# Kernel optimization log

Measured on AMD Instinct MI355X. Metric: run time of the kernel, lower is better.

Reference implementation:

```python
import jax, jax.numpy as jnp
import numpy as np

B, C, D, O = 64, 64, 512, 256
N_REG, G = 8, 8  # 8 regions of 8 channels


def setup_inputs() -> dict:
    key = jax.random.key(0)
    ks = jax.random.split(key, 9)
    std = 0.02  # init_weights_classify: normal(0, 0.02) for Linear weights, zero bias
    x = jax.random.normal(ks[0], (B, C, D), dtype=jnp.float32)
    region_indices = jnp.arange(C, dtype=jnp.int32).reshape(N_REG, G)
    # attn_fc: Linear(2D -> D), ReLU, Linear(D -> 1)
    W1 = jax.random.normal(ks[1], (2 * D, D), dtype=jnp.float32) * std
    b1 = jnp.zeros((D,), jnp.float32)
    W2 = jax.random.normal(ks[2], (D, 1), dtype=jnp.float32) * std
    b2 = jnp.zeros((1,), jnp.float32)
    # gcn1: Linear(D -> D); gcn2: Linear(D -> O)
    Wg1 = jax.random.normal(ks[3], (D, D), dtype=jnp.float32) * std
    bg1 = jnp.zeros((D,), jnp.float32)
    Wg2 = jax.random.normal(ks[4], (D, O), dtype=jnp.float32) * std
    bg2 = jnp.zeros((O,), jnp.float32)
    return {"x": x, "W1": W1, "b1": b1, "W2": W2, "b2": b2,
            "Wg1": Wg1, "bg1": bg1, "Wg2": Wg2, "bg2": bg2,
            "region_indices": region_indices}


def _leaky_relu02(z):
    return jnp.where(z >= 0, z, 0.2 * z)


def reference(x, W1, b1, W2, b2, Wg1, bg1, Wg2, bg2, region_indices):
    Bb, Cc, Dd = x.shape
    n_reg, g = region_indices.shape
    # channel -> region id; mask[i,j] = same region and i != j
    rid = jnp.zeros((Cc,), jnp.int32).at[region_indices.reshape(-1)].set(
        jnp.repeat(jnp.arange(n_reg, dtype=jnp.int32), g))
    idx = jnp.arange(Cc)
    mask = (rid[:, None] == rid[None, :]) & (idx[:, None] != idx[None, :])  # [C, C]
    # attn_fc on cat(x_i, x_j): split first linear to avoid [B,C,C,2D] concat
    a = x @ W1[:Dd]   # [B, C, D]
    bpart = x @ W1[Dd:]  # [B, C, D]
    h = jax.nn.relu(a[:, :, None, :] + bpart[:, None, :, :] + b1)  # [B, C, C, D]
    scores = jnp.einsum('bijd,do->bij', h, W2) + b2[0]  # [B, C, C]
    scores = jnp.where(mask[None, :, :], scores, -jnp.inf)
    adj = jax.nn.softmax(scores, axis=-1)  # [B, C, C]
    # gcn1: adj @ x -> Linear -> LeakyReLU(0.2); residual mix
    m1 = jnp.einsum('bij,bjd->bid', adj, x)
    x1 = _leaky_relu02(m1 @ Wg1 + bg1)
    x1 = 0.5 * x1 + 0.5 * x
    # gcn2
    m2 = jnp.einsum('bij,bjd->bid', adj, x1)
    out = _leaky_relu02(m2 @ Wg2 + bg2)  # [B, C, O]
    return out
```

## Files before the change

### kernel.cpp

```cpp
#include <hip/hip_runtime.h>
#include <math.h>

#define B_   64
#define C_   64
#define D_   512
#define O_   256
#define G_   8
#define M_   4096

typedef __attribute__((ext_vector_type(8))) short s16x8;
typedef __attribute__((ext_vector_type(4))) float f32x4;
typedef unsigned short u16;
typedef unsigned int   u32;

__device__ __forceinline__ float bf2f(u16 u) { return __uint_as_float(((u32)u) << 16); }
__device__ __forceinline__ u16 f2bf(float f) {
    u32 u = __float_as_uint(f);
    return (u16)((u + 0x7FFFu + ((u >> 16) & 1u)) >> 16);
}
__device__ __forceinline__ void gload16(const void* g, void* l) {
    __builtin_amdgcn_global_load_lds((const __attribute__((address_space(1))) u32*)g,
                                     (__attribute__((address_space(3))) u32*)l, 16, 0, 0);
}

__global__ __launch_bounds__(256)
void prep_kernel(const float* __restrict__ x, u16* __restrict__ x_bf,
                 const float* __restrict__ W1, u16* __restrict__ W1t,
                 const float* __restrict__ Wg1, u16* __restrict__ Wg1t,
                 const float* __restrict__ Wg2, u16* __restrict__ Wg2t,
                 const int* __restrict__ region_indices, int* __restrict__ rid)
{
    __shared__ float tile[32][33];
    const int bx = blockIdx.x, tid = threadIdx.x;
    if (bx < 1024) {
        size_t i = ((size_t)bx * 256 + tid) * 8;
        const float4* p = (const float4*)(x + i);
        float4 v0 = p[0], v1 = p[1];
        s16x8 o;
        o[0] = (short)f2bf(v0.x); o[1] = (short)f2bf(v0.y);
        o[2] = (short)f2bf(v0.z); o[3] = (short)f2bf(v0.w);
        o[4] = (short)f2bf(v1.x); o[5] = (short)f2bf(v1.y);
        o[6] = (short)f2bf(v1.z); o[7] = (short)f2bf(v1.w);
        *(s16x8*)(x_bf + i) = o;
        return;
    }
    if (bx >= 1920) {
        if (tid < 64) rid[region_indices[tid]] = tid >> 3;
        return;
    }
    const float* src; u16* dst; int k0, n0, nsrc, obase;
    if (bx < 1536) {
        int idx = bx - 1024, h = idx >> 8, t = idx & 255;
        int tn = t & 15, tk = t >> 4;
        src = W1 + (size_t)h * 512 * 512; dst = W1t; obase = h * 512;
        k0 = tk * 32; n0 = tn * 32; nsrc = 512;
    } else if (bx < 1792) {
        int t = bx - 1536, tn = t & 15, tk = t >> 4;
        src = Wg1; dst = Wg1t; obase = 0;
        k0 = tk * 32; n0 = tn * 32; nsrc = 512;
    } else {
        int t = bx - 1792, tn = t & 7, tk = t >> 3;
        src = Wg2; dst = Wg2t; obase = 0;
        k0 = tk * 32; n0 = tn * 32; nsrc = 256;
    }
    int tx = tid & 31, ty = tid >> 5;
    #pragma unroll
    for (int j = 0; j < 4; j++)
        tile[ty + j * 8][tx] = src[(size_t)(k0 + ty + j * 8) * nsrc + n0 + tx];
    __syncthreads();
    #pragma unroll
    for (int j = 0; j < 4; j++)
        dst[(size_t)(obase + n0 + ty + j * 8) * 512 + k0 + tx] = f2bf(tile[tx][ty + j * 8]);
}

template<int BM, int BN, int EPI>
__global__ __launch_bounds__(256)
void mfma_gemm(const u16* __restrict__ A, const u16* __restrict__ Bt,
               u16* __restrict__ Obf0, u16* __restrict__ Obf1,
               const float* __restrict__ bias, const float* __restrict__ resid,
               float* __restrict__ Of)
{
    constexpr int K = 512, BK = 64, NT = K / BK;
    constexpr int MR = BM / 32, NR = BN / 32;
    constexpr int CA = BM / 32, CB = BN / 32;

    __shared__ __align__(16) u16 As[2][BM * BK];
    __shared__ __align__(16) u16 Bs[2][BN * BK];

    const int tid = threadIdx.x;
    const int lane = tid & 63;
    const int w = tid >> 6, wr = w >> 1, wc = w & 1;
    const int lr = lane & 15, lq = lane >> 4;
    const int m0 = blockIdx.y * BM, n0 = blockIdx.x * BN;

    const int sr  = tid >> 3;
    const int ss  = tid & 7;
    const int gsl = ss ^ (sr & 7);

    f32x4 acc[MR][NR] = {};

    auto stage = [&](int buf, int kt) {
        #pragma unroll
        for (int ch = 0; ch < CA; ch++)
            gload16(A + (size_t)(m0 + ch * 32 + sr) * K + kt + gsl * 8,
                    &As[buf][ch * 2048 + tid * 8]);
        #pragma unroll
        for (int ch = 0; ch < CB; ch++)
            gload16(Bt + (size_t)(n0 + ch * 32 + sr) * K + kt + gsl * 8,
                    &Bs[buf][ch * 2048 + tid * 8]);
    };

    stage(0, 0);
    int cur = 0;
    for (int t = 0; t < NT; t++) {
        __syncthreads();
        if (t + 1 < NT) stage(cur ^ 1, (t + 1) * BK);
        const u16* as = As[cur]; const u16* bs = Bs[cur];
        #pragma unroll
        for (int ks = 0; ks < 2; ks++) {
            s16x8 af[MR], bfv[NR];
            #pragma unroll
            for (int m = 0; m < MR; m++) {
                int r = wr * (BM / 2) + m * 16 + lr;
                af[m] = *(const s16x8*)(as + r * 64 + (((ks * 4 + lq) ^ (r & 7)) * 8));
            }
            #pragma unroll
            for (int n = 0; n < NR; n++) {
                int r = wc * (BN / 2) + n * 16 + lr;
                bfv[n] = *(const s16x8*)(bs + r * 64 + (((ks * 4 + lq) ^ (r & 7)) * 8));
            }
            #pragma unroll
            for (int m = 0; m < MR; m++)
                #pragma unroll
                for (int n = 0; n < NR; n++)
                    acc[m][n] = __builtin_amdgcn_mfma_f32_16x16x32_bf16(af[m], bfv[n], acc[m][n], 0, 0, 0);
        }
        cur ^= 1;
    }

    #pragma unroll
    for (int m = 0; m < MR; m++) {
        #pragma unroll
        for (int n = 0; n < NR; n++) {
            #pragma unroll
            for (int j = 0; j < 4; j++) {
                int row = m0 + wr * (BM / 2) + m * 16 + lq * 4 + j;
                int col = n0 + wc * (BN / 2) + n * 16 + lr;
                float v = acc[m][n][j];
                if (EPI == 0) {
                    if (col < 512) Obf0[(size_t)row * 512 + col] = f2bf(v);
                    else           Obf1[(size_t)row * 512 + col - 512] = f2bf(v);
                } else if (EPI == 1) {
                    v += bias[col];
                    v = (v >= 0.f) ? v : 0.2f * v;
                    v = 0.5f * v + 0.5f * resid[(size_t)row * 512 + col];
                    Obf0[(size_t)row * 512 + col] = f2bf(v);
                } else {
                    v += bias[col];
                    v = (v >= 0.f) ? v : 0.2f * v;
                    Of[(size_t)row * 256 + col] = v;
                }
            }
        }
    }
}

__global__ __launch_bounds__(256)
void scores_m1_kernel(const u16* __restrict__ a, const u16* __restrict__ bpart,
                      const float* __restrict__ x,
                      const float* __restrict__ b1, const float* __restrict__ W2,
                      const float* __restrict__ b2,
                      const int* __restrict__ region_indices, const int* __restrict__ rid,
                      float* __restrict__ adjw, u16* __restrict__ m1)
{
    const int lane = threadIdx.x & 63;
    const int bi = blockIdx.x * 4 + (threadIdx.x >> 6);
    const int b = bi >> 6, i = bi & 63;
    const int r = rid[i];
    int members[8];
    #pragma unroll
    for (int m = 0; m < 8; m++) members[m] = region_indices[r * 8 + m];

    const int d0 = lane * 8;
    s16x8 av8 = *(const s16x8*)(a + (size_t)bi * 512 + d0);
    float4 b1a = *(const float4*)(b1 + d0), b1b = *(const float4*)(b1 + d0 + 4);
    float4 w2a = *(const float4*)(W2 + d0), w2b = *(const float4*)(W2 + d0 + 4);
    float ai[8] = { bf2f((u16)av8[0]) + b1a.x, bf2f((u16)av8[1]) + b1a.y,
                    bf2f((u16)av8[2]) + b1a.z, bf2f((u16)av8[3]) + b1a.w,
                    bf2f((u16)av8[4]) + b1b.x, bf2f((u16)av8[5]) + b1b.y,
                    bf2f((u16)av8[6]) + b1b.z, bf2f((u16)av8[7]) + b1b.w };
    float w2v[8] = { w2a.x, w2a.y, w2a.z, w2a.w, w2b.x, w2b.y, w2b.z, w2b.w };

    s16x8 bv[8];
    #pragma unroll
    for (int m = 0; m < 8; m++)
        bv[m] = *(const s16x8*)(bpart + ((size_t)(b * 64 + members[m])) * 512 + d0);

    float p[8];
    #pragma unroll
    for (int m = 0; m < 8; m++) {
        float s = 0.f;
        #pragma unroll
        for (int t = 0; t < 8; t++) {
            float h = ai[t] + bf2f((u16)bv[m][t]);
            s += fmaxf(h, 0.f) * w2v[t];
        }
        p[m] = s;
    }
    #pragma unroll
    for (int off = 32; off >= 1; off >>= 1)
        #pragma unroll
        for (int m = 0; m < 8; m++) p[m] += __shfl_xor(p[m], off);

    const float bias2 = b2[0];
    float scmax = -INFINITY;
    #pragma unroll
    for (int m = 0; m < 8; m++) {
        p[m] = (members[m] == i) ? -INFINITY : p[m] + bias2;
        scmax = fmaxf(scmax, p[m]);
    }
    float esum = 0.f;
    #pragma unroll
    for (int m = 0; m < 8; m++) {
        p[m] = (members[m] == i) ? 0.f : __expf(p[m] - scmax);
        esum += p[m];
    }
    const float inv = 1.f / esum;

    float accv[8] = {};
    #pragma unroll
    for (int m = 0; m < 8; m++) {
        p[m] *= inv;
        if (members[m] != i) {
            const float4* xp = (const float4*)(x + ((size_t)(b * 64 + members[m])) * 512 + d0);
            float4 xa = xp[0], xb = xp[1];
            accv[0] += p[m] * xa.x; accv[1] += p[m] * xa.y;
            accv[2] += p[m] * xa.z; accv[3] += p[m] * xa.w;
            accv[4] += p[m] * xb.x; accv[5] += p[m] * xb.y;
            accv[6] += p[m] * xb.z; accv[7] += p[m] * xb.w;
        }
    }
    s16x8 o;
    #pragma unroll
    for (int t = 0; t < 8; t++) o[t] = (short)f2bf(accv[t]);
    *(s16x8*)(m1 + (size_t)bi * 512 + d0) = o;
    if (lane < 8) adjw[(size_t)bi * 8 + lane] = p[lane];
}

__global__ __launch_bounds__(256)
void m2_kernel(const u16* __restrict__ x1,
               const int* __restrict__ region_indices, const int* __restrict__ rid,
               const float* __restrict__ adjw, u16* __restrict__ m2)
{
    const int lane = threadIdx.x & 63;
    const int bi = blockIdx.x * 4 + (threadIdx.x >> 6);
    const int b = bi >> 6, i = bi & 63;
    const int r = rid[i];
    const int d0 = lane * 8;
    float accv[8] = {};
    #pragma unroll
    for (int m = 0; m < 8; m++) {
        float wm = adjw[(size_t)bi * 8 + m];
        int j = region_indices[r * 8 + m];
        s16x8 v = *(const s16x8*)(x1 + ((size_t)(b * 64 + j)) * 512 + d0);
        #pragma unroll
        for (int t = 0; t < 8; t++) accv[t] += wm * bf2f((u16)v[t]);
    }
    s16x8 o;
    #pragma unroll
    for (int t = 0; t < 8; t++) o[t] = (short)f2bf(accv[t]);
    *(s16x8*)(m2 + (size_t)bi * 512 + d0) = o;
}

extern "C" void kernel_launch(void* const* d_in, const int* in_sizes, int n_in,
                              void* d_out, int out_size, void* d_ws, size_t ws_size,
                              hipStream_t stream) {
    const float* x    = (const float*)d_in[0];
    const float* W1   = (const float*)d_in[1];
    const float* b1   = (const float*)d_in[2];
    const float* W2   = (const float*)d_in[3];
    const float* b2   = (const float*)d_in[4];
    const float* Wg1  = (const float*)d_in[5];
    const float* bg1  = (const float*)d_in[6];
    const float* Wg2  = (const float*)d_in[7];
    const float* bg2  = (const float*)d_in[8];
    const int* region_indices = (const int*)d_in[9];
    float* out = (float*)d_out;

    char* ws = (char*)d_ws;
    const size_t MB = 1024 * 1024;
    u16*   x_bf  = (u16*)(ws);
    u16*   W1t   = (u16*)(ws + 4 * MB);
    u16*   Wg1t  = (u16*)(ws + 5 * MB);
    u16*   Wg2t  = (u16*)(ws + 5 * MB + 512 * 1024);
    u16*   a_bf  = (u16*)(ws + 6 * MB);
    u16*   bp_bf = (u16*)(ws + 10 * MB);
    u16*   m1_bf = (u16*)(ws + 14 * MB);
    u16*   x1_bf = a_bf;
    u16*   m2_bf = bp_bf;
    float* adjw  = (float*)(ws + 18 * MB);
    int*   rid   = (int*)(ws + 18 * MB + 256 * 1024);

    prep_kernel<<<1921, 256, 0, stream>>>(x, x_bf, W1, W1t, Wg1, Wg1t, Wg2, Wg2t,
                                          region_indices, rid);

    mfma_gemm<128, 64, 0><<<dim3(16, 32), 256, 0, stream>>>(
        x_bf, W1t, a_bf, bp_bf, nullptr, nullptr, nullptr);

    scores_m1_kernel<<<1024, 256, 0, stream>>>(a_bf, bp_bf, x, b1, W2, b2,
                                               region_indices, rid, adjw, m1_bf);

    mfma_gemm<64, 64, 1><<<dim3(8, 64), 256, 0, stream>>>(
        m1_bf, Wg1t, x1_bf, nullptr, bg1, x, nullptr);

    m2_kernel<<<1024, 256, 0, stream>>>(x1_bf, region_indices, rid, adjw, m2_bf);

    mfma_gemm<64, 64, 2><<<dim3(4, 64), 256, 0, stream>>>(
        m2_bf, Wg2t, nullptr, nullptr, bg2, nullptr, out);
}
```

Before: 120.5 us.

## Fuse gcn1 GEMM with m2 aggregation, stage batch rows in LDS, add XCD swizzle

The gcn1 GEMM epilogue now writes its 64x64 x1 tile to LDS and performs the region-wise adjacency aggregation for m2 in the same kernel. This removes the separate m2 kernel and the x1 round trip through global memory. The scores kernel now loads a whole batch's bpart and bf16 x into LDS (128KB) and loops over rows, and region ids are computed inside the kernels rather than in prep. GEMM blocks are remapped for XCD locality. In exchange, the large LDS footprint lowers scores-kernel occupancy, and m1 aggregation now reads bf16 x instead of fp32, which lowers precision.

```diff
diff --git a/kernel.cpp b/kernel.cpp
--- a/kernel.cpp
+++ b/kernel.cpp
@@ -22,13 +22,20 @@
     __builtin_amdgcn_global_load_lds((const __attribute__((address_space(1))) u32*)g,
                                      (__attribute__((address_space(3))) u32*)l, 16, 0, 0);
 }
+__device__ __forceinline__ void xcd_swz(int& bx, int& by) {
+    int nx = (int)gridDim.x;
+    int L = bx + by * nx;
+    int nwg = nx * (int)gridDim.y;
+    int nid = (L & 7) * (nwg >> 3) + (L >> 3);
+    bx = nid & (nx - 1);
+    by = nid / nx;
+}
 
 __global__ __launch_bounds__(256)
 void prep_kernel(const float* __restrict__ x, u16* __restrict__ x_bf,
                  const float* __restrict__ W1, u16* __restrict__ W1t,
                  const float* __restrict__ Wg1, u16* __restrict__ Wg1t,
-                 const float* __restrict__ Wg2, u16* __restrict__ Wg2t,
-                 const int* __restrict__ region_indices, int* __restrict__ rid)
+                 const float* __restrict__ Wg2, u16* __restrict__ Wg2t)
 {
     __shared__ float tile[32][33];
     const int bx = blockIdx.x, tid = threadIdx.x;
@@ -44,24 +51,19 @@
         *(s16x8*)(x_bf + i) = o;
         return;
     }
-    if (bx >= 1920) {
-        if (tid < 64) rid[region_indices[tid]] = tid >> 3;
-        return;
-    }
     const float* src; u16* dst; int k0, n0, nsrc, obase;
     if (bx < 1536) {
         int idx = bx - 1024, h = idx >> 8, t = idx & 255;
-        int tn = t & 15, tk = t >> 4;
         src = W1 + (size_t)h * 512 * 512; dst = W1t; obase = h * 512;
-        k0 = tk * 32; n0 = tn * 32; nsrc = 512;
+        k0 = (t >> 4) * 32; n0 = (t & 15) * 32; nsrc = 512;
     } else if (bx < 1792) {
-        int t = bx - 1536, tn = t & 15, tk = t >> 4;
+        int t = bx - 1536;
         src = Wg1; dst = Wg1t; obase = 0;
-        k0 = tk * 32; n0 = tn * 32; nsrc = 512;
+        k0 = (t >> 4) * 32; n0 = (t & 15) * 32; nsrc = 512;
     } else {
-        int t = bx - 1792, tn = t & 7, tk = t >> 3;
+        int t = bx - 1792;
         src = Wg2; dst = Wg2t; obase = 0;
-        k0 = tk * 32; n0 = tn * 32; nsrc = 256;
+        k0 = (t >> 3) * 32; n0 = (t & 7) * 32; nsrc = 256;
     }
     int tx = tid & 31, ty = tid >> 5;
     #pragma unroll
@@ -77,8 +79,7 @@
 __global__ __launch_bounds__(256)
 void mfma_gemm(const u16* __restrict__ A, const u16* __restrict__ Bt,
                u16* __restrict__ Obf0, u16* __restrict__ Obf1,
-               const float* __restrict__ bias, const float* __restrict__ resid,
-               float* __restrict__ Of)
+               const float* __restrict__ bias, float* __restrict__ Of)
 {
     constexpr int K = 512, BK = 64, NT = K / BK;
     constexpr int MR = BM / 32, NR = BN / 32;
@@ -91,7 +92,9 @@
     const int lane = tid & 63;
     const int w = tid >> 6, wr = w >> 1, wc = w & 1;
     const int lr = lane & 15, lq = lane >> 4;
-    const int m0 = blockIdx.y * BM, n0 = blockIdx.x * BN;
+    int bx = blockIdx.x, by = blockIdx.y;
+    xcd_swz(bx, by);
+    const int m0 = by * BM, n0 = bx * BN;
 
     const int sr  = tid >> 3;
     const int ss  = tid & 7;
@@ -150,11 +153,6 @@
                 if (EPI == 0) {
                     if (col < 512) Obf0[(size_t)row * 512 + col] = f2bf(v);
                     else           Obf1[(size_t)row * 512 + col - 512] = f2bf(v);
-                } else if (EPI == 1) {
-                    v += bias[col];
-                    v = (v >= 0.f) ? v : 0.2f * v;
-                    v = 0.5f * v + 0.5f * resid[(size_t)row * 512 + col];
-                    Obf0[(size_t)row * 512 + col] = f2bf(v);
                 } else {
                     v += bias[col];
                     v = (v >= 0.f) ? v : 0.2f * v;
@@ -166,110 +164,214 @@
 }
 
 __global__ __launch_bounds__(256)
-void scores_m1_kernel(const u16* __restrict__ a, const u16* __restrict__ bpart,
-                      const float* __restrict__ x,
+void scores_m1_kernel(const u16* __restrict__ a_bf, const u16* __restrict__ bp_bf,
+                      const u16* __restrict__ x_bf,
                       const float* __restrict__ b1, const float* __restrict__ W2,
                       const float* __restrict__ b2,
-                      const int* __restrict__ region_indices, const int* __restrict__ rid,
+                      const int* __restrict__ region_indices,
                       float* __restrict__ adjw, u16* __restrict__ m1)
 {
-    const int lane = threadIdx.x & 63;
-    const int bi = blockIdx.x * 4 + (threadIdx.x >> 6);
-    const int b = bi >> 6, i = bi & 63;
-    const int r = rid[i];
-    int members[8];
-    #pragma unroll
-    for (int m = 0; m < 8; m++) members[m] = region_indices[r * 8 + m];
+    __shared__ __align__(16) u16 bp_lds[64 * 512];
+    __shared__ __align__(16) u16 x_lds[64 * 512];
+    __shared__ int ri_lds[64];
+    __shared__ int rid_lds[64];
+
+    int L = blockIdx.x;
+    int nid = ((L & 7) << 5) + (L >> 3);
+    const int b = nid >> 2, q = nid & 3;
+    const int tid = threadIdx.x, lane = tid & 63, w = tid >> 6;
+
+    #pragma unroll
+    for (int it = 0; it < 16; it++) {
+        gload16(bp_bf + (size_t)b * 32768 + it * 2048 + tid * 8, bp_lds + it * 2048 + tid * 8);
+        gload16(x_bf  + (size_t)b * 32768 + it * 2048 + tid * 8, x_lds  + it * 2048 + tid * 8);
+    }
+    if (tid < 64) {
+        int c = region_indices[tid];
+        ri_lds[tid] = c;
+        rid_lds[c] = tid >> 3;
+    }
 
     const int d0 = lane * 8;
-    s16x8 av8 = *(const s16x8*)(a + (size_t)bi * 512 + d0);
     float4 b1a = *(const float4*)(b1 + d0), b1b = *(const float4*)(b1 + d0 + 4);
     float4 w2a = *(const float4*)(W2 + d0), w2b = *(const float4*)(W2 + d0 + 4);
-    float ai[8] = { bf2f((u16)av8[0]) + b1a.x, bf2f((u16)av8[1]) + b1a.y,
-                    bf2f((u16)av8[2]) + b1a.z, bf2f((u16)av8[3]) + b1a.w,
-                    bf2f((u16)av8[4]) + b1b.x, bf2f((u16)av8[5]) + b1b.y,
-                    bf2f((u16)av8[6]) + b1b.z, bf2f((u16)av8[7]) + b1b.w };
+    float b1v[8] = { b1a.x, b1a.y, b1a.z, b1a.w, b1b.x, b1b.y, b1b.z, b1b.w };
     float w2v[8] = { w2a.x, w2a.y, w2a.z, w2a.w, w2b.x, w2b.y, w2b.z, w2b.w };
-
-    s16x8 bv[8];
-    #pragma unroll
-    for (int m = 0; m < 8; m++)
-        bv[m] = *(const s16x8*)(bpart + ((size_t)(b * 64 + members[m])) * 512 + d0);
-
-    float p[8];
-    #pragma unroll
-    for (int m = 0; m < 8; m++) {
-        float s = 0.f;
-        #pragma unroll
-        for (int t = 0; t < 8; t++) {
-            float h = ai[t] + bf2f((u16)bv[m][t]);
-            s += fmaxf(h, 0.f) * w2v[t];
-        }
-        p[m] = s;
-    }
-    #pragma unroll
-    for (int off = 32; off >= 1; off >>= 1)
-        #pragma unroll
-        for (int m = 0; m < 8; m++) p[m] += __shfl_xor(p[m], off);
-
     const float bias2 = b2[0];
-    float scmax = -INFINITY;
-    #pragma unroll
-    for (int m = 0; m < 8; m++) {
-        p[m] = (members[m] == i) ? -INFINITY : p[m] + bias2;
-        scmax = fmaxf(scmax, p[m]);
-    }
-    float esum = 0.f;
-    #pragma unroll
-    for (int m = 0; m < 8; m++) {
-        p[m] = (members[m] == i) ? 0.f : __expf(p[m] - scmax);
-        esum += p[m];
-    }
-    const float inv = 1.f / esum;
-
-    float accv[8] = {};
-    #pragma unroll
-    for (int m = 0; m < 8; m++) {
-        p[m] *= inv;
-        if (members[m] != i) {
-            const float4* xp = (const float4*)(x + ((size_t)(b * 64 + members[m])) * 512 + d0);
-            float4 xa = xp[0], xb = xp[1];
-            accv[0] += p[m] * xa.x; accv[1] += p[m] * xa.y;
-            accv[2] += p[m] * xa.z; accv[3] += p[m] * xa.w;
-            accv[4] += p[m] * xb.x; accv[5] += p[m] * xb.y;
-            accv[6] += p[m] * xb.z; accv[7] += p[m] * xb.w;
-        }
-    }
-    s16x8 o;
-    #pragma unroll
-    for (int t = 0; t < 8; t++) o[t] = (short)f2bf(accv[t]);
-    *(s16x8*)(m1 + (size_t)bi * 512 + d0) = o;
-    if (lane < 8) adjw[(size_t)bi * 8 + lane] = p[lane];
+
+    __syncthreads();
+
+    for (int rr = 0; rr < 4; rr++) {
+        const int i = q * 16 + w * 4 + rr;
+        const int bi = b * 64 + i;
+        const int r = rid_lds[i];
+        int mem[8];
+        #pragma unroll
+        for (int m = 0; m < 8; m++) mem[m] = ri_lds[r * 8 + m];
+
+        s16x8 a8 = *(const s16x8*)(a_bf + (size_t)bi * 512 + d0);
+        float ai[8];
+        #pragma unroll
+        for (int t = 0; t < 8; t++) ai[t] = bf2f((u16)a8[t]) + b1v[t];
+
+        float p[8];
+        #pragma unroll
+        for (int m = 0; m < 8; m++) {
+            s16x8 bv = *(const s16x8*)(bp_lds + mem[m] * 512 + d0);
+            float s = 0.f;
+            #pragma unroll
+            for (int t = 0; t < 8; t++) {
+                float h = ai[t] + bf2f((u16)bv[t]);
+                s += fmaxf(h, 0.f) * w2v[t];
+            }
+            p[m] = s;
+        }
+        #pragma unroll
+        for (int off = 32; off >= 1; off >>= 1)
+            #pragma unroll
+            for (int m = 0; m < 8; m++) p[m] += __shfl_xor(p[m], off);
+
+        float scmax = -INFINITY;
+        #pragma unroll
+        for (int m = 0; m < 8; m++) {
+            p[m] = (mem[m] == i) ? -INFINITY : p[m] + bias2;
+            scmax = fmaxf(scmax, p[m]);
+        }
+        float esum = 0.f;
+        #pragma unroll
+        for (int m = 0; m < 8; m++) {
+            p[m] = (mem[m] == i) ? 0.f : __expf(p[m] - scmax);
+            esum += p[m];
+        }
+        const float inv = 1.f / esum;
+
+        float accv[8] = {};
+        #pragma unroll
+        for (int m = 0; m < 8; m++) {
+            p[m] *= inv;
+            s16x8 xv = *(const s16x8*)(x_lds + mem[m] * 512 + d0);
+            #pragma unroll
+            for (int t = 0; t < 8; t++) accv[t] += p[m] * bf2f((u16)xv[t]);
+        }
+        s16x8 o;
+        #pragma unroll
+        for (int t = 0; t < 8; t++) o[t] = (short)f2bf(accv[t]);
+        *(s16x8*)(m1 + (size_t)bi * 512 + d0) = o;
+        if (lane < 8) adjw[(size_t)bi * 8 + lane] = p[lane];
+    }
 }
 
 __global__ __launch_bounds__(256)
-void m2_kernel(const u16* __restrict__ x1,
-               const int* __restrict__ region_indices, const int* __restrict__ rid,
-               const float* __restrict__ adjw, u16* __restrict__ m2)
+void gemm2_m2_kernel(const u16* __restrict__ A, const u16* __restrict__ Bt,
+                     const float* __restrict__ bias, const float* __restrict__ xres,
+                     const float* __restrict__ adjw, const int* __restrict__ region_indices,
+                     u16* __restrict__ m2)
 {
-    const int lane = threadIdx.x & 63;
-    const int bi = blockIdx.x * 4 + (threadIdx.x >> 6);
-    const int b = bi >> 6, i = bi & 63;
-    const int r = rid[i];
-    const int d0 = lane * 8;
-    float accv[8] = {};
+    constexpr int K = 512, BK = 64, NT = K / BK;
+    __shared__ __align__(16) u16 As[2][64 * 64];
+    __shared__ __align__(16) u16 Bs[2][64 * 64];
+    __shared__ __align__(16) u16 x1s[64 * 72];
+    __shared__ int ri_lds[64];
+    __shared__ int rid_lds[64];
+
+    const int tid = threadIdx.x;
+    const int lane = tid & 63;
+    const int w = tid >> 6, wr = w >> 1, wc = w & 1;
+    const int lr = lane & 15, lq = lane >> 4;
+    int bx = blockIdx.x, by = blockIdx.y;
+    xcd_swz(bx, by);
+    const int b = by, n0 = bx * 64;
+    const int m0 = b * 64;
+
+    const int sr = tid >> 3, ss = tid & 7;
+    const int gsl = ss ^ (sr & 7);
+
+    if (tid < 64) {
+        int c = region_indices[tid];
+        ri_lds[tid] = c;
+        rid_lds[c] = tid >> 3;
+    }
+
+    f32x4 acc[2][2] = {};
+
+    auto stage = [&](int buf, int kt) {
+        #pragma unroll
+        for (int ch = 0; ch < 2; ch++)
+            gload16(A + (size_t)(m0 + ch * 32 + sr) * K + kt + gsl * 8,
+                    &As[buf][ch * 2048 + tid * 8]);
+        #pragma unroll
+        for (int ch = 0; ch < 2; ch++)
+            gload16(Bt + (size_t)(n0 + ch * 32 + sr) * K + kt + gsl * 8,
+                    &Bs[buf][ch * 2048 + tid * 8]);
+    };
+
+    stage(0, 0);
+    int cur = 0;
+    for (int t = 0; t < NT; t++) {
+        __syncthreads();
+        if (t + 1 < NT) stage(cur ^ 1, (t + 1) * BK);
+        const u16* as = As[cur]; const u16* bs = Bs[cur];
+        #pragma unroll
+        for (int ks = 0; ks < 2; ks++) {
+            s16x8 af[2], bfv[2];
+            #pragma unroll
+            for (int m = 0; m < 2; m++) {
+                int r = wr * 32 + m * 16 + lr;
+                af[m] = *(const s16x8*)(as + r * 64 + (((ks * 4 + lq) ^ (r & 7)) * 8));
+            }
+            #pragma unroll
+            for (int n = 0; n < 2; n++) {
+                int r = wc * 32 + n * 16 + lr;
+                bfv[n] = *(const s16x8*)(bs + r * 64 + (((ks * 4 + lq) ^ (r & 7)) * 8));
+            }
+            #pragma unroll
+            for (int m = 0; m < 2; m++)
+                #pragma unroll
+                for (int n = 0; n < 2; n++)
+                    acc[m][n] = __builtin_amdgcn_mfma_f32_16x16x32_bf16(af[m], bfv[n], acc[m][n], 0, 0, 0);
+        }
+        cur ^= 1;
+    }
+
+    #pragma unroll
+    for (int m = 0; m < 2; m++) {
+        #pragma unroll
+        for (int n = 0; n < 2; n++) {
+            #pragma unroll
+            for (int j = 0; j < 4; j++) {
+                int lrow = wr * 32 + m * 16 + lq * 4 + j;
+                int lcol = wc * 32 + n * 16 + lr;
+                float v = acc[m][n][j] + bias[n0 + lcol];
+                v = (v >= 0.f) ? v : 0.2f * v;
+                v = 0.5f * v + 0.5f * xres[(size_t)(m0 + lrow) * 512 + n0 + lcol];
+                x1s[lrow * 72 + lcol] = f2bf(v);
+            }
+        }
+    }
+    __syncthreads();
+
+    const int i = tid >> 2, cb = tid & 3, c0 = cb * 16;
+    const int bi = m0 + i;
+    const int r = rid_lds[i];
+    float acc2[16] = {};
     #pragma unroll
     for (int m = 0; m < 8; m++) {
         float wm = adjw[(size_t)bi * 8 + m];
-        int j = region_indices[r * 8 + m];
-        s16x8 v = *(const s16x8*)(x1 + ((size_t)(b * 64 + j)) * 512 + d0);
-        #pragma unroll
-        for (int t = 0; t < 8; t++) accv[t] += wm * bf2f((u16)v[t]);
-    }
-    s16x8 o;
-    #pragma unroll
-    for (int t = 0; t < 8; t++) o[t] = (short)f2bf(accv[t]);
-    *(s16x8*)(m2 + (size_t)bi * 512 + d0) = o;
+        int j = ri_lds[r * 8 + m];
+        #pragma unroll
+        for (int cc = 0; cc < 2; cc++) {
+            s16x8 v = *(const s16x8*)(x1s + j * 72 + c0 + cc * 8);
+            #pragma unroll
+            for (int t = 0; t < 8; t++) acc2[cc * 8 + t] += wm * bf2f((u16)v[t]);
+        }
+    }
+    #pragma unroll
+    for (int cc = 0; cc < 2; cc++) {
+        s16x8 o;
+        #pragma unroll
+        for (int t = 0; t < 8; t++) o[t] = (short)f2bf(acc2[cc * 8 + t]);
+        *(s16x8*)(m2 + (size_t)bi * 512 + n0 + c0 + cc * 8) = o;
+    }
 }
 
 extern "C" void kernel_launch(void* const* d_in, const int* in_sizes, int n_in,
@@ -296,25 +398,20 @@
     u16*   a_bf  = (u16*)(ws + 6 * MB);
     u16*   bp_bf = (u16*)(ws + 10 * MB);
     u16*   m1_bf = (u16*)(ws + 14 * MB);
-    u16*   x1_bf = a_bf;
-    u16*   m2_bf = bp_bf;
-    float* adjw  = (float*)(ws + 18 * MB);
-    int*   rid   = (int*)(ws + 18 * MB + 256 * 1024);
-
-    prep_kernel<<<1921, 256, 0, stream>>>(x, x_bf, W1, W1t, Wg1, Wg1t, Wg2, Wg2t,
-                                          region_indices, rid);
+    u16*   m2_bf = (u16*)(ws + 18 * MB);
+    float* adjw  = (float*)(ws + 22 * MB);
+
+    prep_kernel<<<1920, 256, 0, stream>>>(x, x_bf, W1, W1t, Wg1, Wg1t, Wg2, Wg2t);
 
     mfma_gemm<128, 64, 0><<<dim3(16, 32), 256, 0, stream>>>(
-        x_bf, W1t, a_bf, bp_bf, nullptr, nullptr, nullptr);
-
-    scores_m1_kernel<<<1024, 256, 0, stream>>>(a_bf, bp_bf, x, b1, W2, b2,
-                                               region_indices, rid, adjw, m1_bf);
-
-    mfma_gemm<64, 64, 1><<<dim3(8, 64), 256, 0, stream>>>(
-        m1_bf, Wg1t, x1_bf, nullptr, bg1, x, nullptr);
-
-    m2_kernel<<<1024, 256, 0, stream>>>(x1_bf, region_indices, rid, adjw, m2_bf);
+        x_bf, W1t, a_bf, bp_bf, nullptr, nullptr);
+
+    scores_m1_kernel<<<256, 256, 0, stream>>>(a_bf, bp_bf, x_bf, b1, W2, b2,
+                                              region_indices, adjw, m1_bf);
+
+    gemm2_m2_kernel<<<dim3(8, 64), 256, 0, stream>>>(
+        m1_bf, Wg1t, bg1, x, adjw, region_indices, m2_bf);
 
     mfma_gemm<64, 64, 2><<<dim3(4, 64), 256, 0, stream>>>(
-        m2_bf, Wg2t, nullptr, nullptr, bg2, nullptr, out);
-}
+        m2_bf, Wg2t, nullptr, nullptr, bg2, out);
+}
```

Measured after the change: 120.3 us. Within noise of the previous version (-0.2%).
